# Kernel tuning notes

Hardware: AMD Instinct MI355X
Metric: run time of the kernel (lower is better)

Reference implementation:

```python
import jax, jax.numpy as jnp
import numpy as np

AFWD = 0.999   # alpha_fwd
ABKW = 0.99    # alpha_bkw
EPS = 1e-05


def setup_inputs() -> dict:
    key = jax.random.key(0)
    B, H, W, C = 32, 64, 64, 256
    x = jax.random.normal(key, (B, H, W, C), dtype=jnp.float32)
    return {
        "x": x,
        "mu0": jnp.zeros((C,), jnp.float32),   # streaming mean  (zeros init)
        "var0": jnp.ones((C,), jnp.float32),   # streaming var   (ones init)
        "u0": jnp.zeros((C,), jnp.float32),    # u control (bwd) (zeros init)
        "v0": jnp.zeros((C,), jnp.float32),    # v control (bwd) (zeros init)
    }


def _fwd_scan(x, mu0, var0):
    """Online Normalization forward: sequential EMA over the batch axis.

    Per sample t (channels-last, stats per channel over spatial dims):
      out_t   = (x_t - mu_{t-1}) / sqrt(var_{t-1} + eps)
      var_t   = a*var_{t-1} + (1-a)*Var[x_t] + a*(1-a)*(E[x_t]-mu_{t-1})^2
      mu_t    = mu_{t-1} + (1-a)*(E[x_t]-mu_{t-1})
    The TF layer accelerates this same recurrence with afpow/abpow convs.
    """
    def step(carry, xt):                      # xt: [H, W, C]
        s_mu, s_var = carry                   # [C], [C]
        scale = jnp.sqrt(s_var + EPS)         # [C]
        out = (xt - s_mu) / scale             # broadcast over H, W
        mu_t = jnp.mean(xt, axis=(0, 1))                      # [C]
        var_t = jnp.mean(jnp.square(xt - mu_t), axis=(0, 1))  # biased var, [C]
        new_var = AFWD * s_var + (1.0 - AFWD) * var_t \
                  + AFWD * (1.0 - AFWD) * jnp.square(mu_t - s_mu)
        new_mu = s_mu + (1.0 - AFWD) * (mu_t - s_mu)
        return (new_mu, new_var), (out, scale)

    (mu_f, var_f), (out, scale) = jax.lax.scan(step, (mu0, var0), x)
    return out, scale, mu_f, var_f


def reference(x, mu0, var0, u0, v0):
    out, _, _, _ = _fwd_scan(x, mu0, var0)
    return out
```

## Files before the change

kernel.cpp:

```cpp
#include <hip/hip_runtime.h>
#include <math.h>

#define AFWD 0.999f
#define EPS  1e-5f

constexpr int B  = 32;
constexpr int HW = 64 * 64;
constexpr int C  = 256;
constexpr int CQ = C / 4;
constexpr int CHUNKS = 32;
constexpr int ROWS_PER_CHUNK = HW / CHUNKS;

__global__ void k_partial(const float4* __restrict__ x4,
                          float4* __restrict__ psum,
                          float4* __restrict__ psq) {
    const int chunk = blockIdx.x;
    const int t     = blockIdx.y;
    const int tid   = threadIdx.x;
    const int cq    = tid & 63;
    const int rs    = tid >> 6;

    float4 s = make_float4(0.f, 0.f, 0.f, 0.f);
    float4 q = make_float4(0.f, 0.f, 0.f, 0.f);

    const int base_row = t * HW + chunk * ROWS_PER_CHUNK;
    #pragma unroll 4
    for (int k = 0; k < ROWS_PER_CHUNK / 4; ++k) {
        const int r = base_row + rs + k * 4;
        const float4 v = x4[(long)r * CQ + cq];
        s.x += v.x; s.y += v.y; s.z += v.z; s.w += v.w;
        q.x += v.x * v.x; q.y += v.y * v.y; q.z += v.z * v.z; q.w += v.w * v.w;
    }

    __shared__ float4 ls[256];
    __shared__ float4 lq[256];
    ls[tid] = s;
    lq[tid] = q;
    __syncthreads();

    if (tid < 64) {
        float4 a0 = ls[tid], a1 = ls[tid + 64], a2 = ls[tid + 128], a3 = ls[tid + 192];
        float4 b0 = lq[tid], b1 = lq[tid + 64], b2 = lq[tid + 128], b3 = lq[tid + 192];
        float4 ts, tq;
        ts.x = a0.x + a1.x + a2.x + a3.x;
        ts.y = a0.y + a1.y + a2.y + a3.y;
        ts.z = a0.z + a1.z + a2.z + a3.z;
        ts.w = a0.w + a1.w + a2.w + a3.w;
        tq.x = b0.x + b1.x + b2.x + b3.x;
        tq.y = b0.y + b1.y + b2.y + b3.y;
        tq.z = b0.z + b1.z + b2.z + b3.z;
        tq.w = b0.w + b1.w + b2.w + b3.w;
        const int o = (t * CHUNKS + chunk) * CQ + tid;
        psum[o] = ts;
        psq[o]  = tq;
    }
}

__global__ void k_reduce(const float* __restrict__ psum,
                         const float* __restrict__ psq,
                         float* __restrict__ mean_t,
                         float* __restrict__ var_t) {
    const int t = blockIdx.x;
    const int c = threadIdx.x;
    float s = 0.f, q = 0.f;
    #pragma unroll
    for (int ch = 0; ch < CHUNKS; ++ch) {
        s += psum[(t * CHUNKS + ch) * C + c];
        q += psq [(t * CHUNKS + ch) * C + c];
    }
    const float inv = 1.0f / (float)HW;
    const float m = s * inv;
    mean_t[t * C + c] = m;
    var_t [t * C + c] = q * inv - m * m;
}

__global__ void k_scan(const float* __restrict__ mu0,
                       const float* __restrict__ var0,
                       const float* __restrict__ mean_t,
                       const float* __restrict__ var_t,
                       float* __restrict__ mu_prev,
                       float* __restrict__ rstd) {
    const int c = threadIdx.x;
    float mu  = mu0[c];
    float var = var0[c];
    #pragma unroll
    for (int t = 0; t < B; ++t) {
        mu_prev[t * C + c] = mu;
        rstd  [t * C + c] = 1.0f / sqrtf(var + EPS);
        const float m  = mean_t[t * C + c];
        const float vt = var_t [t * C + c];
        const float d  = m - mu;
        var = AFWD * var + (1.0f - AFWD) * vt + AFWD * (1.0f - AFWD) * d * d;
        mu  = mu + (1.0f - AFWD) * d;
    }
}

__global__ void k_norm(const float4* __restrict__ x4,
                       const float4* __restrict__ mu_prev4,
                       const float4* __restrict__ rstd4,
                       float4* __restrict__ out4) {
    const int t   = blockIdx.y;
    const int tid = threadIdx.x;
    const int cq  = tid & 63;

    const float4 mu = mu_prev4[t * CQ + cq];
    const float4 rs = rstd4  [t * CQ + cq];

    const long base = (long)t * (HW * CQ) + (long)blockIdx.x * (256 * 16);
    #pragma unroll 4
    for (int k = 0; k < 16; ++k) {
        const long i = base + k * 256 + tid;
        const float4 v = x4[i];
        float4 o;
        o.x = (v.x - mu.x) * rs.x;
        o.y = (v.y - mu.y) * rs.y;
        o.z = (v.z - mu.z) * rs.z;
        o.w = (v.w - mu.w) * rs.w;
        out4[i] = o;
    }
}

extern "C" void kernel_launch(void* const* d_in, const int* in_sizes, int n_in,
                              void* d_out, int out_size, void* d_ws, size_t ws_size,
                              hipStream_t stream) {
    const float* x   = (const float*)d_in[0];
    const float* mu0 = (const float*)d_in[1];
    const float* var0= (const float*)d_in[2];

    float* out = (float*)d_out;

    char* ws = (char*)d_ws;
    float4* psum    = (float4*)(ws);
    float4* psq     = (float4*)(ws + (1u << 20));
    float*  mean_t  = (float*) (ws + (2u << 20));
    float*  var_t   = (float*) (ws + (2u << 20) + (32u << 10));
    float*  mu_prev = (float*) (ws + (2u << 20) + (64u << 10));
    float*  rstd    = (float*) (ws + (2u << 20) + (96u << 10));

    const float4* x4 = (const float4*)x;

    k_partial<<<dim3(CHUNKS, B), 256, 0, stream>>>(x4, psum, psq);

    k_reduce<<<dim3(B), 256, 0, stream>>>((const float*)psum, (const float*)psq,
                                          mean_t, var_t);

    k_scan<<<dim3(1), 256, 0, stream>>>(mu0, var0, mean_t, var_t, mu_prev, rstd);

    k_norm<<<dim3(HW * CQ / (256 * 16), B), 256, 0, stream>>>(
        x4, (const float4*)mu_prev, (const float4*)rstd, (float4*)out);
}
```

Measured before the change: 267.6 us.

## Fuse reduce and scan into partial and norm kernels using atomic accumulation

Replaces the four-kernel pipeline (partial sums, reduce, single-block scan, normalize) with two kernels plus a memset. Partial sums go straight into per-sample channel totals via atomicAdd, and each normalize block recomputes the EMA recurrence up to its own sample. This removes two launches and the serial single-block scan. In exchange it adds atomics, a memset, redundant per-block scan work of up to 31 steps, and floating-point summation order that now depends on scheduling.

```diff
diff --git a/kernel.cpp b/kernel.cpp
--- a/kernel.cpp
+++ b/kernel.cpp
@@ -9,25 +9,26 @@
 constexpr int C  = 256;
 constexpr int CQ = C / 4;
 constexpr int CHUNKS = 32;
-constexpr int ROWS_PER_CHUNK = HW / CHUNKS;
+constexpr int RPC = HW / CHUNKS;
 
-__global__ void k_partial(const float4* __restrict__ x4,
-                          float4* __restrict__ psum,
-                          float4* __restrict__ psq) {
-    const int chunk = blockIdx.x;
-    const int t     = blockIdx.y;
+__global__ void __launch_bounds__(256)
+k1_partial(const float4* __restrict__ x4,
+           float* __restrict__ accum_s,
+           float* __restrict__ accum_q) {
+    const int blk   = blockIdx.x;
+    const int t     = blk >> 5;
+    const int chunk = blk & 31;
     const int tid   = threadIdx.x;
     const int cq    = tid & 63;
     const int rs    = tid >> 6;
 
+    const long base = (long)(t * HW + chunk * RPC) * CQ;
+
     float4 s = make_float4(0.f, 0.f, 0.f, 0.f);
     float4 q = make_float4(0.f, 0.f, 0.f, 0.f);
-
-    const int base_row = t * HW + chunk * ROWS_PER_CHUNK;
     #pragma unroll 4
-    for (int k = 0; k < ROWS_PER_CHUNK / 4; ++k) {
-        const int r = base_row + rs + k * 4;
-        const float4 v = x4[(long)r * CQ + cq];
+    for (int k = 0; k < RPC / 4; ++k) {
+        const float4 v = x4[base + (long)(rs + k * 4) * CQ + cq];
         s.x += v.x; s.y += v.y; s.z += v.z; s.w += v.w;
         q.x += v.x * v.x; q.y += v.y * v.y; q.z += v.z * v.z; q.w += v.w * v.w;
     }
@@ -38,84 +39,63 @@
     lq[tid] = q;
     __syncthreads();
 
-    if (tid < 64) {
-        float4 a0 = ls[tid], a1 = ls[tid + 64], a2 = ls[tid + 128], a3 = ls[tid + 192];
-        float4 b0 = lq[tid], b1 = lq[tid + 64], b2 = lq[tid + 128], b3 = lq[tid + 192];
-        float4 ts, tq;
-        ts.x = a0.x + a1.x + a2.x + a3.x;
-        ts.y = a0.y + a1.y + a2.y + a3.y;
-        ts.z = a0.z + a1.z + a2.z + a3.z;
-        ts.w = a0.w + a1.w + a2.w + a3.w;
-        tq.x = b0.x + b1.x + b2.x + b3.x;
-        tq.y = b0.y + b1.y + b2.y + b3.y;
-        tq.z = b0.z + b1.z + b2.z + b3.z;
-        tq.w = b0.w + b1.w + b2.w + b3.w;
-        const int o = (t * CHUNKS + chunk) * CQ + tid;
-        psum[o] = ts;
-        psq[o]  = tq;
+    const int c    = tid;
+    const int cq2  = c >> 2;
+    const int comp = c & 3;
+    float ssum = 0.f, qsum = 0.f;
+    #pragma unroll
+    for (int k = 0; k < 4; ++k) {
+        ssum += ((const float*)&ls[k * 64 + cq2])[comp];
+        qsum += ((const float*)&lq[k * 64 + cq2])[comp];
     }
+    atomicAdd(&accum_s[t * C + c], ssum);
+    atomicAdd(&accum_q[t * C + c], qsum);
 }
 
-__global__ void k_reduce(const float* __restrict__ psum,
-                         const float* __restrict__ psq,
-                         float* __restrict__ mean_t,
-                         float* __restrict__ var_t) {
-    const int t = blockIdx.x;
-    const int c = threadIdx.x;
-    float s = 0.f, q = 0.f;
-    #pragma unroll
-    for (int ch = 0; ch < CHUNKS; ++ch) {
-        s += psum[(t * CHUNKS + ch) * C + c];
-        q += psq [(t * CHUNKS + ch) * C + c];
-    }
+__global__ void __launch_bounds__(256)
+k2_norm(const float4* __restrict__ x4,
+        const float* __restrict__ mu0,
+        const float* __restrict__ var0,
+        const float* __restrict__ accum_s,
+        const float* __restrict__ accum_q,
+        float4* __restrict__ out4) {
+    const int blk   = blockIdx.x;
+    const int t     = blk >> 5;
+    const int chunk = blk & 31;
+    const int tid   = threadIdx.x;
+
+    float mu  = mu0[tid];
+    float var = var0[tid];
     const float inv = 1.0f / (float)HW;
-    const float m = s * inv;
-    mean_t[t * C + c] = m;
-    var_t [t * C + c] = q * inv - m * m;
-}
-
-__global__ void k_scan(const float* __restrict__ mu0,
-                       const float* __restrict__ var0,
-                       const float* __restrict__ mean_t,
-                       const float* __restrict__ var_t,
-                       float* __restrict__ mu_prev,
-                       float* __restrict__ rstd) {
-    const int c = threadIdx.x;
-    float mu  = mu0[c];
-    float var = var0[c];
-    #pragma unroll
-    for (int t = 0; t < B; ++t) {
-        mu_prev[t * C + c] = mu;
-        rstd  [t * C + c] = 1.0f / sqrtf(var + EPS);
-        const float m  = mean_t[t * C + c];
-        const float vt = var_t [t * C + c];
+    for (int tt = 0; tt < t; ++tt) {
+        const float m  = accum_s[tt * C + tid] * inv;
+        const float vt = accum_q[tt * C + tid] * inv - m * m;
         const float d  = m - mu;
         var = AFWD * var + (1.0f - AFWD) * vt + AFWD * (1.0f - AFWD) * d * d;
         mu  = mu + (1.0f - AFWD) * d;
     }
-}
 
-__global__ void k_norm(const float4* __restrict__ x4,
-                       const float4* __restrict__ mu_prev4,
-                       const float4* __restrict__ rstd4,
-                       float4* __restrict__ out4) {
-    const int t   = blockIdx.y;
-    const int tid = threadIdx.x;
-    const int cq  = tid & 63;
+    __shared__ float smu[C];
+    __shared__ float srs[C];
+    smu[tid] = mu;
+    srs[tid] = 1.0f / sqrtf(var + EPS);
+    __syncthreads();
 
-    const float4 mu = mu_prev4[t * CQ + cq];
-    const float4 rs = rstd4  [t * CQ + cq];
+    const int cq = tid & 63;
+    const int rs = tid >> 6;
+    const float4 mu4 = ((const float4*)smu)[cq];
+    const float4 rs4 = ((const float4*)srs)[cq];
 
-    const long base = (long)t * (HW * CQ) + (long)blockIdx.x * (256 * 16);
+    const long base = (long)(t * HW + chunk * RPC) * CQ;
     #pragma unroll 4
-    for (int k = 0; k < 16; ++k) {
-        const long i = base + k * 256 + tid;
+    for (int k = 0; k < RPC / 4; ++k) {
+        const long i = base + (long)(rs + k * 4) * CQ + cq;
         const float4 v = x4[i];
         float4 o;
-        o.x = (v.x - mu.x) * rs.x;
-        o.y = (v.y - mu.y) * rs.y;
-        o.z = (v.z - mu.z) * rs.z;
-        o.w = (v.w - mu.w) * rs.w;
+        o.x = (v.x - mu4.x) * rs4.x;
+        o.y = (v.y - mu4.y) * rs4.y;
+        o.z = (v.z - mu4.z) * rs4.z;
+        o.w = (v.w - mu4.w) * rs4.w;
         out4[i] = o;
     }
 }
@@ -123,29 +103,18 @@
 extern "C" void kernel_launch(void* const* d_in, const int* in_sizes, int n_in,
                               void* d_out, int out_size, void* d_ws, size_t ws_size,
                               hipStream_t stream) {
-    const float* x   = (const float*)d_in[0];
-    const float* mu0 = (const float*)d_in[1];
-    const float* var0= (const float*)d_in[2];
+    const float4* x4   = (const float4*)d_in[0];
+    const float*  mu0  = (const float*)d_in[1];
+    const float*  var0 = (const float*)d_in[2];
+    float4* out4 = (float4*)d_out;
 
-    float* out = (float*)d_out;
+    float* accum_s = (float*)d_ws;
+    float* accum_q = accum_s + B * C;
 
-    char* ws = (char*)d_ws;
-    float4* psum    = (float4*)(ws);
-    float4* psq     = (float4*)(ws + (1u << 20));
-    float*  mean_t  = (float*) (ws + (2u << 20));
-    float*  var_t   = (float*) (ws + (2u << 20) + (32u << 10));
-    float*  mu_prev = (float*) (ws + (2u << 20) + (64u << 10));
-    float*  rstd    = (float*) (ws + (2u << 20) + (96u << 10));
+    hipMemsetAsync(d_ws, 0, 2 * B * C * sizeof(float), stream);
 
-    const float4* x4 = (const float4*)x;
+    k1_partial<<<dim3(B * CHUNKS), 256, 0, stream>>>(x4, accum_s, accum_q);
 
-    k_partial<<<dim3(CHUNKS, B), 256, 0, stream>>>(x4, psum, psq);
-
-    k_reduce<<<dim3(B), 256, 0, stream>>>((const float*)psum, (const float*)psq,
-                                          mean_t, var_t);
-
-    k_scan<<<dim3(1), 256, 0, stream>>>(mu0, var0, mean_t, var_t, mu_prev, rstd);
-
-    k_norm<<<dim3(HW * CQ / (256 * 16), B), 256, 0, stream>>>(
-        x4, (const float4*)mu_prev, (const float4*)rstd, (float4*)out);
+    k2_norm<<<dim3(B * CHUNKS), 256, 0, stream>>>(x4, mu0, var0,
+                                                  accum_s, accum_q, out4);
 }
```

New measurement: 261.3 us. 2.4% less time.
